# Kernel optimization log

Hardware: AMD Instinct MI355X
Metric: run time of the kernel (lower is better)

Reference implementation:

```python
import jax, jax.numpy as jnp
import numpy as np

B, N, E, F, FE = 4, 10000, 160000, 128, 16  # batch, nodes, edges, filters(=node feat dim), edge feat dim
EPS = 1e-3  # keras LayerNormalization default epsilon


def layernorm(x, gamma, beta):
    mu = jnp.mean(x, axis=-1, keepdims=True)
    var = jnp.mean(jnp.square(x - mu), axis=-1, keepdims=True)
    return (x - mu) * jax.lax.rsqrt(var + EPS) * gamma + beta


def setup_inputs() -> dict:
    key = jax.random.key(0)
    ks = jax.random.split(key, 8)
    nodes = jax.random.normal(ks[0], (B, N, F), dtype=jnp.float32)
    edge_features = jax.random.normal(ks[1], (B, E, FE), dtype=jnp.float32)
    edges = jax.random.randint(ks[2], (B, E, 2), 0, N, dtype=jnp.int32)
    edge_weights = jax.random.uniform(ks[3], (B, E, 1), dtype=jnp.float32)
    edge_dropout = jnp.ones((B, E, 2), dtype=jnp.float32)
    W_msg = jax.random.normal(ks[4], (2 * F + FE, F), dtype=jnp.float32) * 0.02
    b_msg = jnp.zeros((F,), jnp.float32)
    g_msg = jnp.ones((F,), jnp.float32)
    beta_msg = jnp.zeros((F,), jnp.float32)
    W_upd = jax.random.normal(ks[5], (2 * F, F), dtype=jnp.float32) * 0.02
    b_upd = jnp.zeros((F,), jnp.float32)
    g_upd = jnp.ones((F,), jnp.float32)
    beta_upd = jnp.zeros((F,), jnp.float32)
    return dict(nodes=nodes, edge_features=edge_features, edges=edges,
                edge_weights=edge_weights, edge_dropout=edge_dropout,
                W_msg=W_msg, b_msg=b_msg, g_msg=g_msg, beta_msg=beta_msg,
                W_upd=W_upd, b_upd=b_upd, g_upd=g_upd, beta_upd=beta_upd)


def reference(nodes, edge_features, edges, edge_weights, edge_dropout,
              W_msg, b_msg, g_msg, beta_msg, W_upd, b_upd, g_upd, beta_upd):
    n = nodes.shape[1]
    # gather both endpoints per edge: [B,E,2,F] -> [B,E,2F]
    gathered = jax.vmap(lambda nd, ed: nd[ed])(nodes, edges)
    msg_in = gathered.reshape(gathered.shape[0], gathered.shape[1], -1)
    msg_in = jnp.concatenate([msg_in, edge_features], axis=-1)
    # message MLP: Dense + GELU + LayerNorm
    h = jnp.einsum('bei,io->beo', msg_in, W_msg) + b_msg
    messages = layernorm(jax.nn.gelu(h, approximate=False), g_msg, beta_msg)
    weighted_messages = messages * edge_weights
    # scatter-sum to destination nodes (edge[:,1]), masked by dropout col 1
    dropped = weighted_messages * edge_dropout[..., 1:2]
    dst = edges[..., 1]
    aggregated = jax.vmap(lambda m, d: jax.ops.segment_sum(m, d, num_segments=n))(dropped, dst)
    # update: concat + Dense + GELU + LayerNorm
    combined = jnp.concatenate([nodes, aggregated], axis=-1)
    u = jnp.einsum('bni,io->bno', combined, W_upd) + b_upd
    updated_nodes = layernorm(jax.nn.gelu(u, approximate=False), g_upd, beta_upd)
    return updated_nodes
```

## Files before the change

kernel.cpp:

```cpp
#include <hip/hip_runtime.h>
#include <hip/hip_bf16.h>
#include <hip/hip_fp16.h>

#define BATCH   4
#define NNODES  10000
#define NEDGES  160000
#define FDIM    128
#define FEDIM   16
#define LNEPS   1e-3f
#define NTOTE   (BATCH * NEDGES)
#define NTOTN   (BATCH * NNODES)

typedef __attribute__((ext_vector_type(8))) short v8s;
typedef __attribute__((ext_vector_type(4))) float v4f;

#define AGG_BYTES   ((size_t)NTOTN * FDIM * 2)
#define CNT_OFF     AGG_BYTES
#define CNT_BYTES   ((size_t)NTOTN * 4)
#define CUR_OFF     (CNT_OFF + CNT_BYTES)
#define P_OFF       (CUR_OFF + CNT_BYTES)
#define P_BYTES     ((size_t)NTOTN * 256 * 2)
#define WTCAT_OFF   (P_OFF + P_BYTES)
#define WTUPD_OFF   (WTCAT_OFF + (size_t)256 * 128 * 2)
#define W3T_OFF     (WTUPD_OFF + (size_t)128 * 256 * 2)
#define REC_OFF     (W3T_OFF + (size_t)128 * 32 * 2)

static __device__ __forceinline__ unsigned short f2bf(float f) {
    __hip_bfloat16 h = __float2bfloat16(f);
    return *reinterpret_cast<unsigned short*>(&h);
}
static __device__ __forceinline__ float bfbits2f(unsigned bits16) {
    return __uint_as_float(bits16 << 16);
}

static __device__ __forceinline__ float gelu_f(float x) {
    float z = 0.7978845608028654f * (x + 0.044715f * x * x * x);
    float e = __expf(2.0f * z);
    float t = 1.0f - 2.0f / (e + 1.0f);
    return 0.5f * x * (1.0f + t);
}

static __device__ __forceinline__ bool is_bf16_mode(const void* gflag) {
    return ((*reinterpret_cast<const unsigned*>(gflag)) & 0xFFFFu) != 0u;
}
static __device__ __forceinline__ float ld_f(const void* p, long i, bool bf) {
    return bf ? (float)reinterpret_cast<const __hip_bfloat16*>(p)[i]
              : reinterpret_cast<const float*>(p)[i];
}
static __device__ __forceinline__ uint4 pack8(const float* p) {
    float4 f0 = *reinterpret_cast<const float4*>(p);
    float4 f1 = *reinterpret_cast<const float4*>(p + 4);
    uint4 o;
    o.x = f2bf(f0.x) | ((unsigned)f2bf(f0.y) << 16);
    o.y = f2bf(f0.z) | ((unsigned)f2bf(f0.w) << 16);
    o.z = f2bf(f1.x) | ((unsigned)f2bf(f1.y) << 16);
    o.w = f2bf(f1.z) | ((unsigned)f2bf(f1.w) << 16);
    return o;
}
static __device__ __forceinline__ uint4 h8_to_bf8(uint4 u) {
    unsigned w[4] = {u.x, u.y, u.z, u.w};
    uint4 o; unsigned r[4];
    #pragma unroll
    for (int q = 0; q < 4; q++) {
        __half lo = *reinterpret_cast<const __half*>(&w[q]);
        unsigned short hib = (unsigned short)(w[q] >> 16);
        __half hi = *reinterpret_cast<const __half*>(&hib);
        r[q] = f2bf(__half2float(lo)) | ((unsigned)f2bf(__half2float(hi)) << 16);
    }
    o.x = r[0]; o.y = r[1]; o.z = r[2]; o.w = r[3];
    return o;
}
static __device__ __forceinline__ uint4 shfl4(uint4 v, int src) {
    uint4 o;
    o.x = (unsigned)__shfl((int)v.x, src);
    o.y = (unsigned)__shfl((int)v.y, src);
    o.z = (unsigned)__shfl((int)v.z, src);
    o.w = (unsigned)__shfl((int)v.w, src);
    return o;
}

#define NCAT (256 * 128)
#define NUPD (128 * 256)
#define NW3  (128 * 32)
__global__ __launch_bounds__(256) void init_kernel(
    const void* __restrict__ Wmsg, const void* __restrict__ Wupd,
    const void* __restrict__ gflag,
    unsigned short* __restrict__ WtCat,
    unsigned short* __restrict__ WtUpd,
    unsigned short* __restrict__ W3t,
    uint4* __restrict__ aggz,
    uint4* __restrict__ cntz) {
    bool bf = is_bf16_mode(gflag);
    int i = blockIdx.x * 256 + threadIdx.x;
    aggz[i] = make_uint4(0, 0, 0, 0);
    if (i < (int)(CNT_BYTES / 16)) cntz[i] = make_uint4(0, 0, 0, 0);
    if (i < NCAT) {
        int n = i >> 7, k = i & 127;
        int src = (n < 128) ? (k * 128 + n) : ((128 + k) * 128 + (n - 128));
        WtCat[i] = bf ? reinterpret_cast<const unsigned short*>(Wmsg)[src]
                      : f2bf(reinterpret_cast<const float*>(Wmsg)[src]);
    } else if (i < NCAT + NUPD) {
        int j = i - NCAT;
        int n = j >> 8, c = j & 255;
        WtUpd[j] = bf ? reinterpret_cast<const unsigned short*>(Wupd)[c * 128 + n]
                      : f2bf(reinterpret_cast<const float*>(Wupd)[c * 128 + n]);
    } else if (i < NCAT + NUPD + NW3) {
        int j = i - NCAT - NUPD;
        int n = j >> 5, k = j & 31;
        W3t[j] = (k < 16) ? (bf ? reinterpret_cast<const unsigned short*>(Wmsg)[(256 + k) * 128 + n]
                                : f2bf(reinterpret_cast<const float*>(Wmsg)[(256 + k) * 128 + n]))
                          : (unsigned short)0;
    }
}

__global__ __launch_bounds__(1024) void scan_kernel(const int* __restrict__ counts,
                                                    int* __restrict__ cursor) {
    __shared__ int wsum[16];
    const int C = 40;
    int tid = threadIdx.x, lane = tid & 63, wave = tid >> 6;
    int lo = tid * C;
    const bool act = (lo < NTOTN);
    int vals[C];
    int s = 0;
    if (act) {
        #pragma unroll
        for (int q = 0; q < C / 4; q++) {
            int4 t4 = *reinterpret_cast<const int4*>(counts + lo + q * 4);
            vals[q * 4 + 0] = t4.x; vals[q * 4 + 1] = t4.y;
            vals[q * 4 + 2] = t4.z; vals[q * 4 + 3] = t4.w;
            s += t4.x + t4.y + t4.z + t4.w;
        }
    }
    int sc = s;
    #pragma unroll
    for (int off = 1; off < 64; off <<= 1) {
        int v = __shfl_up(sc, off);
        if (lane >= off) sc += v;
    }
    if (lane == 63) wsum[wave] = sc;
    __syncthreads();
    if (wave == 0 && lane < 16) {
        int t = wsum[lane];
        #pragma unroll
        for (int off = 1; off < 16; off <<= 1) {
            int v = __shfl_up(t, off);
            if (lane >= off) t += v;
        }
        wsum[lane] = t;
    }
    __syncthreads();
    int run = (wave > 0 ? wsum[wave - 1] : 0) + (sc - s);
    if (act) {
        #pragma unroll
        for (int q = 0; q < C / 4; q++) {
            int4 o;
            o.x = run; run += vals[q * 4 + 0];
            o.y = run; run += vals[q * 4 + 1];
            o.z = run; run += vals[q * 4 + 2];
            o.w = run; run += vals[q * 4 + 3];
            *reinterpret_cast<int4*>(cursor + lo + q * 4) = o;
        }
    }
}

__global__ __launch_bounds__(256) void sort_scatter(
    const int*  __restrict__ edges,
    const void* __restrict__ ew,
    const void* __restrict__ ed,
    const void* __restrict__ efeat,
    const void* __restrict__ gflag,
    int*        __restrict__ cursor,
    uint4*      __restrict__ rec4)
{
    const bool bf = is_bf16_mode(gflag);
    int gid = blockIdx.x * 256 + threadIdx.x;
    const int lane = threadIdx.x & 63, k = lane & 3, g4 = lane & ~3;
    int b = gid / NEDGES;
    long be = gid;
    int2 e = reinterpret_cast<const int2*>(edges)[gid];
    float w = ld_f(ew, be, bf) * ld_f(ed, be * 2 + 1, bf);
    uint4 R0, R1;
    if (bf) {
        const unsigned short* ep = reinterpret_cast<const unsigned short*>(efeat) + be * FEDIM;
        R0 = *reinterpret_cast<const uint4*>(ep);
        R1 = *reinterpret_cast<const uint4*>(ep + 8);
    } else {
        const float* ep = reinterpret_cast<const float*>(efeat) + be * FEDIM;
        R0 = pack8(ep);
        R1 = pack8(ep + 8);
    }
    uint4 R2 = make_uint4((unsigned)(b * NNODES + e.x),
                          (unsigned)(b * NNODES + e.y),
                          __float_as_uint(w),
                          (unsigned)gid);
    int pos = atomicAdd(&cursor[b * NNODES + e.y], 1);

    #pragma unroll
    for (int j = 0; j < 4; j++) {
        int src = g4 + j;
        uint4 a0 = shfl4(R0, src);
        uint4 a1 = shfl4(R1, src);
        uint4 a2 = shfl4(R2, src);
        int   pj = __shfl(pos, src);
        uint4 wv = (k == 0) ? a0 : (k == 1) ? a1 : (k == 2) ? a2 : make_uint4(0, 0, 0, 0);
        rec4[(size_t)pj * 4 + k] = wv;
    }
}

__global__ __launch_bounds__(256) void pg_kernel(
    const void* __restrict__ nodes,
    const void* __restrict__ bmsg,
    const void* __restrict__ gflag,
    const unsigned short* __restrict__ Wt,
    const int*  __restrict__ edges,
    int*        __restrict__ counts,
    unsigned short*       __restrict__ P)
{
    const bool bf = is_bf16_mode(gflag);
    __shared__ unsigned short sW[128 * 40];
    __shared__ unsigned short sA[128 * 40];

    const int tid  = threadIdx.x;
    const int lane = tid & 63, wave = tid >> 6;
    const int c    = lane & 15, quad = lane >> 4;
    const int row0 = blockIdx.x * 128;
    const int half = blockIdx.y;
    const int NROWS = BATCH * NNODES;

    if (half == 0) {
        #pragma unroll
        for (int k = 0; k < 8; k++) {
            int g = blockIdx.x * 2048 + k * 256 + tid;
            if (g < NTOTE) {
                int2 e = reinterpret_cast<const int2*>(edges)[g];
                atomicAdd(&counts[(g / NEDGES) * NNODES + e.y], 1);
            }
        }
    }

    float bcol[8];
    #pragma unroll
    for (int nt = 0; nt < 8; nt++)
        bcol[nt] = (half == 0) ? ld_f(bmsg, nt * 16 + c, bf) : 0.f;

    v4f acc[2][8];
    #pragma unroll
    for (int mt = 0; mt < 2; mt++)
        #pragma unroll
        for (int nt = 0; nt < 8; nt++) { v4f z = {0.f, 0.f, 0.f, 0.f}; acc[mt][nt] = z; }

    for (int ks = 0; ks < 4; ks++) {
        #pragma unroll
        for (int q = tid; q < 512; q += 256) {
            int n = q >> 2, part = q & 3;
            *reinterpret_cast<uint4*>(&sW[n * 40 + part * 8]) =
                *reinterpret_cast<const uint4*>(Wt + (half * 128 + n) * 128 + ks * 32 + part * 8);
        }
        #pragma unroll
        for (int q = tid; q < 512; q += 256) {
            int t = q >> 2, part = q & 3;
            int row = row0 + t; if (row >= NROWS) row = NROWS - 1;
            long off = (size_t)row * FDIM + ks * 32 + part * 8;
            uint4 v = bf ? *reinterpret_cast<const uint4*>(reinterpret_cast<const unsigned short*>(nodes) + off)
                         : pack8(reinterpret_cast<const float*>(nodes) + off);
            *reinterpret_cast<uint4*>(&sA[t * 40 + part * 8]) = v;
        }
        __syncthreads();

        v8s a0 = *reinterpret_cast<const v8s*>(&sA[(wave * 32 + c) * 40 + quad * 8]);
        v8s a1 = *reinterpret_cast<const v8s*>(&sA[(wave * 32 + 16 + c) * 40 + quad * 8]);
        #pragma unroll
        for (int nt = 0; nt < 8; nt++) {
            v8s bfr = *reinterpret_cast<const v8s*>(&sW[(nt * 16 + c) * 40 + quad * 8]);
            acc[0][nt] = __builtin_amdgcn_mfma_f32_16x16x32_bf16(a0, bfr, acc[0][nt], 0, 0, 0);
            acc[1][nt] = __builtin_amdgcn_mfma_f32_16x16x32_bf16(a1, bfr, acc[1][nt], 0, 0, 0);
        }
        __syncthreads();
    }

    #pragma unroll
    for (int mt = 0; mt < 2; mt++)
        #pragma unroll
        for (int r = 0; r < 4; r++) {
            int row = row0 + wave * 32 + mt * 16 + quad * 4 + r;
            if (row < NROWS) {
                float v[8];
                #pragma unroll
                for (int nt = 0; nt < 8; nt++) v[nt] = acc[mt][nt][r] + bcol[nt];
                uint4 o;
                o.x = f2bf(v[0]) | ((unsigned)f2bf(v[1]) << 16);
                o.y = f2bf(v[2]) | ((unsigned)f2bf(v[3]) << 16);
                o.z = f2bf(v[4]) | ((unsigned)f2bf(v[5]) << 16);
                o.w = f2bf(v[6]) | ((unsigned)f2bf(v[7]) << 16);
                *reinterpret_cast<uint4*>(P + (size_t)row * 256 + half * 128 + c * 8) = o;
            }
        }
}

__global__ __launch_bounds__(256) void edge_kernel(
    const unsigned short* __restrict__ P,
    const uint4*          __restrict__ rec4,
    const unsigned short* __restrict__ W3t,
    const void* __restrict__ gmsg,
    const void* __restrict__ betamsg,
    __half*     __restrict__ agg)
{
    const bool bf = is_bf16_mode(gmsg);
    const int tid  = threadIdx.x;
    const int lane = tid & 63, wave = tid >> 6;
    const int c    = lane & 15, quad = lane >> 4;
    const int we0  = blockIdx.x * 128 + wave * 32;

    float gcol[8], becol[8];
    #pragma unroll
    for (int nt = 0; nt < 8; nt++) {
        gcol[nt]  = ld_f(gmsg, nt * 16 + c, bf);
        becol[nt] = ld_f(betamsg, nt * 16 + c, bf);
    }

    v8s bfrag[8];
    #pragma unroll
    for (int nt = 0; nt < 8; nt++)
        bfrag[nt] = *reinterpret_cast<const v8s*>(W3t + (nt * 16 + c) * 32 + quad * 8);

    v4f acc[2][8];
    #pragma unroll
    for (int mt = 0; mt < 2; mt++)
        #pragma unroll
        for (int nt = 0; nt < 8; nt++) { v4f z = {0.f, 0.f, 0.f, 0.f}; acc[mt][nt] = z; }

    #pragma unroll
    for (int mt = 0; mt < 2; mt++) {
        v8s a = {0, 0, 0, 0, 0, 0, 0, 0};
        if (quad < 2) {
            int slot = we0 + ((c >> 2) << 3) + mt * 4 + (c & 3);
            uint4 u = rec4[(size_t)slot * 4 + quad];
            a = *reinterpret_cast<v8s*>(&u);
        }
        #pragma unroll
        for (int nt = 0; nt < 8; nt++)
            acc[mt][nt] = __builtin_amdgcn_mfma_f32_16x16x32_bf16(a, bfrag[nt], acc[mt][nt], 0, 0, 0);
    }

    const bool even = !(c & 1);
    float racc[8];
    int cur = -1;

    auto flushv = [&](int dstrow) {
        __half* aout = agg + (size_t)dstrow * FDIM;
        #pragma unroll
        for (int np = 0; np < 4; np++) {
            int nt = np * 2;
            float t0 = __shfl_xor(racc[nt], 1);
            float t1 = __shfl_xor(racc[nt + 1], 1);
            __half2 v = even ? __floats2half2_rn(racc[nt], t0)
                             : __floats2half2_rn(t1, racc[nt + 1]);
            int hoff = even ? (nt * 16 + c) : ((nt + 1) * 16 + c - 1);
            unsafeAtomicAdd(reinterpret_cast<__half2*>(aout + hoff), v);
        }
    };

    #pragma unroll
    for (int mt = 0; mt < 2; mt++) {
        uint4 H[4];
        #pragma unroll
        for (int r = 0; r < 4; r++)
            H[r] = rec4[(size_t)(we0 + quad * 8 + mt * 4 + r) * 4 + 2];
        uint4 U1[4], U2[4];
        #pragma unroll
        for (int r = 0; r < 4; r++) {
            U1[r] = *reinterpret_cast<const uint4*>(P + (size_t)H[r].x * 256 + c * 8);
            U2[r] = *reinterpret_cast<const uint4*>(P + (size_t)H[r].y * 256 + 128 + c * 8);
        }
        #pragma unroll
        for (int r = 0; r < 4; r++) {
            unsigned w1[4] = {U1[r].x, U1[r].y, U1[r].z, U1[r].w};
            unsigned w2[4] = {U2[r].x, U2[r].y, U2[r].z, U2[r].w};
            float h[8];
            #pragma unroll
            for (int q = 0; q < 4; q++) {
                h[q * 2]     = bfbits2f(w1[q] & 0xFFFFu) + bfbits2f(w2[q] & 0xFFFFu) + acc[mt][q * 2][r];
                h[q * 2 + 1] = __uint_as_float(w1[q] & 0xFFFF0000u) + __uint_as_float(w2[q] & 0xFFFF0000u)
                               + acc[mt][q * 2 + 1][r];
            }
            float s = 0.f, sq = 0.f;
            #pragma unroll
            for (int nt = 0; nt < 8; nt++) {
                float g = gelu_f(h[nt]);
                h[nt] = g; s += g; sq += g * g;
            }
            #pragma unroll
            for (int off = 1; off < 16; off <<= 1) {
                s  += __shfl_xor(s, off);
                sq += __shfl_xor(sq, off);
            }
            float mu  = s * (1.0f / 128.0f);
            float var = sq * (1.0f / 128.0f) - mu * mu;
            float rs  = rsqrtf(var + LNEPS);
            float wgt = __uint_as_float(H[r].z);
            int d = (int)H[r].y;
            if (d != cur) {
                if (cur >= 0) flushv(cur);
                cur = d;
                #pragma unroll
                for (int nt = 0; nt < 8; nt++)
                    racc[nt] = ((h[nt] - mu) * rs * gcol[nt] + becol[nt]) * wgt;
            } else {
                #pragma unroll
                for (int nt = 0; nt < 8; nt++)
                    racc[nt] += ((h[nt] - mu) * rs * gcol[nt] + becol[nt]) * wgt;
            }
        }
    }
    flushv(cur);
}

__global__ __launch_bounds__(256) void upd_kernel(
    const void* __restrict__ nodes,
    const __half* __restrict__ agg,
    const unsigned short* __restrict__ Wt,
    const void* __restrict__ bupd,
    const void* __restrict__ gupd,
    const void* __restrict__ beupd,
    void*       __restrict__ out)
{
    const bool bf = is_bf16_mode(gupd);
    __shared__ unsigned short sW[128 * 40];
    __shared__ unsigned short sA[64 * 40];

    const int tid  = threadIdx.x;
    const int lane = tid & 63, wave = tid >> 6;
    const int c    = lane & 15, quad = lane >> 4;
    const int row0 = blockIdx.x * 64;

    float bcol[8], gcol[8], becol[8];
    #pragma unroll
    for (int nt = 0; nt < 8; nt++) {
        int col = nt * 16 + c;
        bcol[nt]  = ld_f(bupd, col, bf);
        gcol[nt]  = ld_f(gupd, col, bf);
        becol[nt] = ld_f(beupd, col, bf);
    }

    v4f acc[8];
    #pragma unroll
    for (int nt = 0; nt < 8; nt++) { v4f z = {0.f, 0.f, 0.f, 0.f}; acc[nt] = z; }

    for (int ks = 0; ks < 8; ks++) {
        #pragma unroll
        for (int q = tid; q < 512; q += 256) {
            int n = q >> 2, part = q & 3;
            *reinterpret_cast<uint4*>(&sW[n * 40 + part * 8]) =
                *reinterpret_cast<const uint4*>(Wt + n * 256 + ks * 32 + part * 8);
        }
        {
            int t = tid >> 2, part = tid & 3;
            int row = row0 + t;
            uint4 v;
            if (ks < 4) {
                long off = (size_t)row * FDIM + ks * 32 + part * 8;
                v = bf ? *reinterpret_cast<const uint4*>(reinterpret_cast<const unsigned short*>(nodes) + off)
                       : pack8(reinterpret_cast<const float*>(nodes) + off);
            } else {
                uint4 u = *reinterpret_cast<const uint4*>(
                    reinterpret_cast<const unsigned short*>(agg) + (size_t)row * FDIM + (ks - 4) * 32 + part * 8);
                v = h8_to_bf8(u);
            }
            *reinterpret_cast<uint4*>(&sA[t * 40 + part * 8]) = v;
        }
        __syncthreads();

        v8s a0 = *reinterpret_cast<const v8s*>(&sA[(wave * 16 + c) * 40 + quad * 8]);
        #pragma unroll
        for (int nt = 0; nt < 8; nt++) {
            v8s bfr = *reinterpret_cast<const v8s*>(&sW[(nt * 16 + c) * 40 + quad * 8]);
            acc[nt] = __builtin_amdgcn_mfma_f32_16x16x32_bf16(a0, bfr, acc[nt], 0, 0, 0);
        }
        __syncthreads();
    }

    float s[4] = {0, 0, 0, 0}, sq[4] = {0, 0, 0, 0};
    #pragma unroll
    for (int nt = 0; nt < 8; nt++) {
        v4f v = acc[nt];
        #pragma unroll
        for (int r = 0; r < 4; r++) {
            float g = gelu_f(v[r] + bcol[nt]);
            v[r] = g;
            s[r] += g; sq[r] += g * g;
        }
        acc[nt] = v;
    }
    #pragma unroll
    for (int off = 1; off < 16; off <<= 1) {
        #pragma unroll
        for (int r = 0; r < 4; r++) {
            s[r]  += __shfl_xor(s[r], off);
            sq[r] += __shfl_xor(sq[r], off);
        }
    }
    #pragma unroll
    for (int r = 0; r < 4; r++) {
        float mu  = s[r] * (1.0f / 128.0f);
        float var = sq[r] * (1.0f / 128.0f) - mu * mu;
        float rs  = rsqrtf(var + LNEPS);
        int row = row0 + wave * 16 + quad * 4 + r;
        #pragma unroll
        for (int nt = 0; nt < 8; nt++) {
            float y = (acc[nt][r] - mu) * rs * gcol[nt] + becol[nt];
            size_t oi = (size_t)row * FDIM + nt * 16 + c;
            if (bf) reinterpret_cast<__hip_bfloat16*>(out)[oi] = __float2bfloat16(y);
            else    reinterpret_cast<float*>(out)[oi] = y;
        }
    }
}

extern "C" void kernel_launch(void* const* d_in, const int* in_sizes, int n_in,
                              void* d_out, int out_size, void* d_ws, size_t ws_size,
                              hipStream_t stream)
{
    const void* nodes   = d_in[0];
    const void* efeat   = d_in[1];
    const int*  edges   = (const int*)d_in[2];
    const void* ew      = d_in[3];
    const void* ed      = d_in[4];
    const void* Wmsg    = d_in[5];
    const void* bmsg    = d_in[6];
    const void* gmsg    = d_in[7];
    const void* betamsg = d_in[8];
    const void* Wupd    = d_in[9];
    const void* bupd    = d_in[10];
    const void* gupd    = d_in[11];
    const void* betaupd = d_in[12];

    char* ws = (char*)d_ws;
    __half* agg          = (__half*)ws;
    int*    counts       = (int*)(ws + CNT_OFF);
    int*    cursor       = (int*)(ws + CUR_OFF);
    unsigned short* P    = (unsigned short*)(ws + P_OFF);
    unsigned short* WtCat= (unsigned short*)(ws + WTCAT_OFF);
    unsigned short* WtUpd= (unsigned short*)(ws + WTUPD_OFF);
    unsigned short* W3t  = (unsigned short*)(ws + W3T_OFF);
    uint4*          rec4 = (uint4*)(ws + REC_OFF);

    init_kernel<<<2500, 256, 0, stream>>>(
        Wmsg, Wupd, gmsg, WtCat, WtUpd, W3t, (uint4*)agg, (uint4*)counts);
    pg_kernel<<<dim3(313, 2), 256, 0, stream>>>(
        nodes, bmsg, gmsg, WtCat, edges, counts, P);
    scan_kernel<<<1, 1024, 0, stream>>>(counts, cursor);
    sort_scatter<<<NTOTE / 256, 256, 0, stream>>>(
        edges, ew, ed, efeat, gmsg, cursor, rec4);
    edge_kernel<<<NTOTE / 128, 256, 0, stream>>>(
        P, rec4, W3t, gmsg, betamsg, agg);
    upd_kernel<<<NTOTN / 64, 256, 0, stream>>>(
        nodes, agg, WtUpd, bupd, gupd, betaupd, d_out);
}
```

Measured before the change: 321.6 us.

## Spread per-node counters four ways, enlarge edge tiles, skip atomics for owned rows

Node counts and cursors are split into four sub-counters per destination node, chosen by thread index, so the counting and sort atomics in pg_kernel and sort_scatter contend less. sort_scatter now writes records directly instead of shuffling them across lanes. edge_kernel handles 512 edges per block, with each quad walking 32 consecutive sorted edges, and uses plain stores instead of atomic adds when a destination run lies entirely inside one quad's range. GELU and rsqrt switch to cheaper rcp/rsq builtins. The scan grows to four times as many entries and rereads its counts instead of caching them in registers; the init_kernel zeroing covers the larger buffer only if its grid is big enough.

```diff
diff --git a/kernel.cpp b/kernel.cpp
--- a/kernel.cpp
+++ b/kernel.cpp
@@ -16,7 +16,7 @@
 
 #define AGG_BYTES   ((size_t)NTOTN * FDIM * 2)
 #define CNT_OFF     AGG_BYTES
-#define CNT_BYTES   ((size_t)NTOTN * 4)
+#define CNT_BYTES   ((size_t)NTOTN * 4 * 4)
 #define CUR_OFF     (CNT_OFF + CNT_BYTES)
 #define P_OFF       (CUR_OFF + CNT_BYTES)
 #define P_BYTES     ((size_t)NTOTN * 256 * 2)
@@ -34,10 +34,11 @@
 }
 
 static __device__ __forceinline__ float gelu_f(float x) {
-    float z = 0.7978845608028654f * (x + 0.044715f * x * x * x);
-    float e = __expf(2.0f * z);
-    float t = 1.0f - 2.0f / (e + 1.0f);
-    return 0.5f * x * (1.0f + t);
+    float x2 = x * x;
+    float z2 = 1.5957691216f * x * __builtin_fmaf(0.044715f, x2, 1.0f);
+    float e  = __expf(z2);
+    float r  = __builtin_amdgcn_rcpf(e + 1.0f);
+    return __builtin_fmaf(-x, r, x);
 }
 
 static __device__ __forceinline__ bool is_bf16_mode(const void* gflag) {
@@ -68,14 +69,6 @@
         r[q] = f2bf(__half2float(lo)) | ((unsigned)f2bf(__half2float(hi)) << 16);
     }
     o.x = r[0]; o.y = r[1]; o.z = r[2]; o.w = r[3];
-    return o;
-}
-static __device__ __forceinline__ uint4 shfl4(uint4 v, int src) {
-    uint4 o;
-    o.x = (unsigned)__shfl((int)v.x, src);
-    o.y = (unsigned)__shfl((int)v.y, src);
-    o.z = (unsigned)__shfl((int)v.z, src);
-    o.w = (unsigned)__shfl((int)v.w, src);
     return o;
 }
 
@@ -113,21 +106,18 @@
     }
 }
 
-__global__ __launch_bounds__(1024) void scan_kernel(const int* __restrict__ counts,
-                                                    int* __restrict__ cursor) {
+__global__ __launch_bounds__(1024) void scan_kernel(const int* __restrict__ counts4,
+                                                    int* __restrict__ cursor4) {
     __shared__ int wsum[16];
-    const int C = 40;
+    const int N4 = NTOTN * 4;
+    const int C = 160;
     int tid = threadIdx.x, lane = tid & 63, wave = tid >> 6;
     int lo = tid * C;
-    const bool act = (lo < NTOTN);
-    int vals[C];
+    const bool act = (lo < N4);
     int s = 0;
     if (act) {
-        #pragma unroll
         for (int q = 0; q < C / 4; q++) {
-            int4 t4 = *reinterpret_cast<const int4*>(counts + lo + q * 4);
-            vals[q * 4 + 0] = t4.x; vals[q * 4 + 1] = t4.y;
-            vals[q * 4 + 2] = t4.z; vals[q * 4 + 3] = t4.w;
+            int4 t4 = *reinterpret_cast<const int4*>(counts4 + lo + q * 4);
             s += t4.x + t4.y + t4.z + t4.w;
         }
     }
@@ -151,14 +141,14 @@
     __syncthreads();
     int run = (wave > 0 ? wsum[wave - 1] : 0) + (sc - s);
     if (act) {
-        #pragma unroll
         for (int q = 0; q < C / 4; q++) {
+            int4 t4 = *reinterpret_cast<const int4*>(counts4 + lo + q * 4);
             int4 o;
-            o.x = run; run += vals[q * 4 + 0];
-            o.y = run; run += vals[q * 4 + 1];
-            o.z = run; run += vals[q * 4 + 2];
-            o.w = run; run += vals[q * 4 + 3];
-            *reinterpret_cast<int4*>(cursor + lo + q * 4) = o;
+            o.x = run; run += t4.x;
+            o.y = run; run += t4.y;
+            o.z = run; run += t4.z;
+            o.w = run; run += t4.w;
+            *reinterpret_cast<int4*>(cursor4 + lo + q * 4) = o;
         }
     }
 }
@@ -169,12 +159,11 @@
     const void* __restrict__ ed,
     const void* __restrict__ efeat,
     const void* __restrict__ gflag,
-    int*        __restrict__ cursor,
+    int*        __restrict__ cursor4,
     uint4*      __restrict__ rec4)
 {
     const bool bf = is_bf16_mode(gflag);
     int gid = blockIdx.x * 256 + threadIdx.x;
-    const int lane = threadIdx.x & 63, k = lane & 3, g4 = lane & ~3;
     int b = gid / NEDGES;
     long be = gid;
     int2 e = reinterpret_cast<const int2*>(edges)[gid];
@@ -189,22 +178,14 @@
         R0 = pack8(ep);
         R1 = pack8(ep + 8);
     }
-    uint4 R2 = make_uint4((unsigned)(b * NNODES + e.x),
-                          (unsigned)(b * NNODES + e.y),
-                          __float_as_uint(w),
-                          (unsigned)gid);
-    int pos = atomicAdd(&cursor[b * NNODES + e.y], 1);
-
-    #pragma unroll
-    for (int j = 0; j < 4; j++) {
-        int src = g4 + j;
-        uint4 a0 = shfl4(R0, src);
-        uint4 a1 = shfl4(R1, src);
-        uint4 a2 = shfl4(R2, src);
-        int   pj = __shfl(pos, src);
-        uint4 wv = (k == 0) ? a0 : (k == 1) ? a1 : (k == 2) ? a2 : make_uint4(0, 0, 0, 0);
-        rec4[(size_t)pj * 4 + k] = wv;
-    }
+    int pos = atomicAdd(&cursor4[((size_t)b * NNODES + e.y) * 4 + (threadIdx.x & 3)], 1);
+    uint4* rp = rec4 + (size_t)pos * 4;
+    rp[0] = R0;
+    rp[1] = R1;
+    rp[2] = make_uint4((unsigned)(b * NNODES + e.x),
+                       (unsigned)(b * NNODES + e.y),
+                       __float_as_uint(w), (unsigned)gid);
+    rp[3] = make_uint4(0, 0, 0, 0);
 }
 
 __global__ __launch_bounds__(256) void pg_kernel(
@@ -213,7 +194,7 @@
     const void* __restrict__ gflag,
     const unsigned short* __restrict__ Wt,
     const int*  __restrict__ edges,
-    int*        __restrict__ counts,
+    int*        __restrict__ counts4,
     unsigned short*       __restrict__ P)
 {
     const bool bf = is_bf16_mode(gflag);
@@ -233,7 +214,7 @@
             int g = blockIdx.x * 2048 + k * 256 + tid;
             if (g < NTOTE) {
                 int2 e = reinterpret_cast<const int2*>(edges)[g];
-                atomicAdd(&counts[(g / NEDGES) * NNODES + e.y], 1);
+                atomicAdd(&counts4[((size_t)(g / NEDGES) * NNODES + e.y) * 4 + (tid & 3)], 1);
             }
         }
     }
@@ -309,7 +290,8 @@
     const int tid  = threadIdx.x;
     const int lane = tid & 63, wave = tid >> 6;
     const int c    = lane & 15, quad = lane >> 4;
-    const int we0  = blockIdx.x * 128 + wave * 32;
+    const int wbase = blockIdx.x * 512 + wave * 128;
+    const int q0    = wbase + quad * 32;
 
     float gcol[8], becol[8];
     #pragma unroll
@@ -323,30 +305,15 @@
     for (int nt = 0; nt < 8; nt++)
         bfrag[nt] = *reinterpret_cast<const v8s*>(W3t + (nt * 16 + c) * 32 + quad * 8);
 
-    v4f acc[2][8];
-    #pragma unroll
-    for (int mt = 0; mt < 2; mt++)
-        #pragma unroll
-        for (int nt = 0; nt < 8; nt++) { v4f z = {0.f, 0.f, 0.f, 0.f}; acc[mt][nt] = z; }
-
-    #pragma unroll
-    for (int mt = 0; mt < 2; mt++) {
-        v8s a = {0, 0, 0, 0, 0, 0, 0, 0};
-        if (quad < 2) {
-            int slot = we0 + ((c >> 2) << 3) + mt * 4 + (c & 3);
-            uint4 u = rec4[(size_t)slot * 4 + quad];
-            a = *reinterpret_cast<v8s*>(&u);
-        }
-        #pragma unroll
-        for (int nt = 0; nt < 8; nt++)
-            acc[mt][nt] = __builtin_amdgcn_mfma_f32_16x16x32_bf16(a, bfrag[nt], acc[mt][nt], 0, 0, 0);
-    }
+    const int prevd = (q0 == 0) ? -1 : (int)rec4[(size_t)(q0 - 1) * 4 + 2].y;
+    const int nextd = (q0 + 32 >= NTOTE) ? -1 : (int)rec4[(size_t)(q0 + 32) * 4 + 2].y;
 
     const bool even = !(c & 1);
     float racc[8];
-    int cur = -1;
-
-    auto flushv = [&](int dstrow) {
+    int  cur = -1;
+    bool owned = true;
+
+    auto flushv = [&](int dstrow, bool plain) {
         __half* aout = agg + (size_t)dstrow * FDIM;
         #pragma unroll
         for (int np = 0; np < 4; np++) {
@@ -356,63 +323,86 @@
             __half2 v = even ? __floats2half2_rn(racc[nt], t0)
                              : __floats2half2_rn(t1, racc[nt + 1]);
             int hoff = even ? (nt * 16 + c) : ((nt + 1) * 16 + c - 1);
-            unsafeAtomicAdd(reinterpret_cast<__half2*>(aout + hoff), v);
+            if (plain) *reinterpret_cast<__half2*>(aout + hoff) = v;
+            else       unsafeAtomicAdd(reinterpret_cast<__half2*>(aout + hoff), v);
         }
     };
 
-    #pragma unroll
-    for (int mt = 0; mt < 2; mt++) {
-        uint4 H[4];
-        #pragma unroll
-        for (int r = 0; r < 4; r++)
-            H[r] = rec4[(size_t)(we0 + quad * 8 + mt * 4 + r) * 4 + 2];
-        uint4 U1[4], U2[4];
-        #pragma unroll
-        for (int r = 0; r < 4; r++) {
-            U1[r] = *reinterpret_cast<const uint4*>(P + (size_t)H[r].x * 256 + c * 8);
-            U2[r] = *reinterpret_cast<const uint4*>(P + (size_t)H[r].y * 256 + 128 + c * 8);
-        }
-        #pragma unroll
-        for (int r = 0; r < 4; r++) {
-            unsigned w1[4] = {U1[r].x, U1[r].y, U1[r].z, U1[r].w};
-            unsigned w2[4] = {U2[r].x, U2[r].y, U2[r].z, U2[r].w};
-            float h[8];
+    for (int g = 0; g < 4; g++) {
+        v4f acc[2][8];
+        #pragma unroll
+        for (int mt = 0; mt < 2; mt++)
             #pragma unroll
-            for (int q = 0; q < 4; q++) {
-                h[q * 2]     = bfbits2f(w1[q] & 0xFFFFu) + bfbits2f(w2[q] & 0xFFFFu) + acc[mt][q * 2][r];
-                h[q * 2 + 1] = __uint_as_float(w1[q] & 0xFFFF0000u) + __uint_as_float(w2[q] & 0xFFFF0000u)
-                               + acc[mt][q * 2 + 1][r];
-            }
-            float s = 0.f, sq = 0.f;
-            #pragma unroll
-            for (int nt = 0; nt < 8; nt++) {
-                float g = gelu_f(h[nt]);
-                h[nt] = g; s += g; sq += g * g;
+            for (int nt = 0; nt < 8; nt++) { v4f z = {0.f, 0.f, 0.f, 0.f}; acc[mt][nt] = z; }
+
+        #pragma unroll
+        for (int mt = 0; mt < 2; mt++) {
+            v8s a = {0, 0, 0, 0, 0, 0, 0, 0};
+            if (quad < 2) {
+                int slot = wbase + (c >> 2) * 32 + g * 8 + mt * 4 + (c & 3);
+                uint4 u = rec4[(size_t)slot * 4 + quad];
+                a = *reinterpret_cast<v8s*>(&u);
             }
             #pragma unroll
-            for (int off = 1; off < 16; off <<= 1) {
-                s  += __shfl_xor(s, off);
-                sq += __shfl_xor(sq, off);
+            for (int nt = 0; nt < 8; nt++)
+                acc[mt][nt] = __builtin_amdgcn_mfma_f32_16x16x32_bf16(a, bfrag[nt], acc[mt][nt], 0, 0, 0);
+        }
+
+        #pragma unroll
+        for (int mt = 0; mt < 2; mt++) {
+            uint4 H[4];
+            #pragma unroll
+            for (int r = 0; r < 4; r++)
+                H[r] = rec4[(size_t)(q0 + g * 8 + mt * 4 + r) * 4 + 2];
+            uint4 U1[4], U2[4];
+            #pragma unroll
+            for (int r = 0; r < 4; r++) {
+                U1[r] = *reinterpret_cast<const uint4*>(P + (size_t)H[r].x * 256 + c * 8);
+                U2[r] = *reinterpret_cast<const uint4*>(P + (size_t)H[r].y * 256 + 128 + c * 8);
             }
-            float mu  = s * (1.0f / 128.0f);
-            float var = sq * (1.0f / 128.0f) - mu * mu;
-            float rs  = rsqrtf(var + LNEPS);
-            float wgt = __uint_as_float(H[r].z);
-            int d = (int)H[r].y;
-            if (d != cur) {
-                if (cur >= 0) flushv(cur);
-                cur = d;
+            #pragma unroll
+            for (int r = 0; r < 4; r++) {
+                unsigned w1[4] = {U1[r].x, U1[r].y, U1[r].z, U1[r].w};
+                unsigned w2[4] = {U2[r].x, U2[r].y, U2[r].z, U2[r].w};
+                float h[8];
                 #pragma unroll
-                for (int nt = 0; nt < 8; nt++)
-                    racc[nt] = ((h[nt] - mu) * rs * gcol[nt] + becol[nt]) * wgt;
-            } else {
+                for (int q = 0; q < 4; q++) {
+                    h[q * 2]     = bfbits2f(w1[q] & 0xFFFFu) + bfbits2f(w2[q] & 0xFFFFu) + acc[mt][q * 2][r];
+                    h[q * 2 + 1] = __uint_as_float(w1[q] & 0xFFFF0000u) + __uint_as_float(w2[q] & 0xFFFF0000u)
+                                   + acc[mt][q * 2 + 1][r];
+                }
+                float s = 0.f, sq = 0.f;
                 #pragma unroll
-                for (int nt = 0; nt < 8; nt++)
-                    racc[nt] += ((h[nt] - mu) * rs * gcol[nt] + becol[nt]) * wgt;
+                for (int nt = 0; nt < 8; nt++) {
+                    float gg = gelu_f(h[nt]);
+                    h[nt] = gg; s += gg; sq += gg * gg;
+                }
+                #pragma unroll
+                for (int off = 1; off < 16; off <<= 1) {
+                    s  += __shfl_xor(s, off);
+                    sq += __shfl_xor(sq, off);
+                }
+                float mu  = s * (1.0f / 128.0f);
+                float var = sq * (1.0f / 128.0f) - mu * mu;
+                float rs  = __builtin_amdgcn_rsqf(var + LNEPS);
+                float wgt = __uint_as_float(H[r].z);
+                int d = (int)H[r].y;
+                if (d != cur) {
+                    if (cur >= 0) { flushv(cur, owned); owned = true; }
+                    else owned = (d != prevd);
+                    cur = d;
+                    #pragma unroll
+                    for (int nt = 0; nt < 8; nt++)
+                        racc[nt] = ((h[nt] - mu) * rs * gcol[nt] + becol[nt]) * wgt;
+                } else {
+                    #pragma unroll
+                    for (int nt = 0; nt < 8; nt++)
+                        racc[nt] += ((h[nt] - mu) * rs * gcol[nt] + becol[nt]) * wgt;
+                }
             }
         }
     }
-    flushv(cur);
+    flushv(cur, owned && (cur != nextd));
 }
 
 __global__ __launch_bounds__(256) void upd_kernel(
@@ -503,7 +493,7 @@
     for (int r = 0; r < 4; r++) {
         float mu  = s[r] * (1.0f / 128.0f);
         float var = sq[r] * (1.0f / 128.0f) - mu * mu;
-        float rs  = rsqrtf(var + LNEPS);
+        float rs  = __builtin_amdgcn_rsqf(var + LNEPS);
         int row = row0 + wave * 16 + quad * 4 + r;
         #pragma unroll
         for (int nt = 0; nt < 8; nt++) {
@@ -535,8 +525,8 @@
 
     char* ws = (char*)d_ws;
     __half* agg          = (__half*)ws;
-    int*    counts       = (int*)(ws + CNT_OFF);
-    int*    cursor       = (int*)(ws + CUR_OFF);
+    int*    counts4      = (int*)(ws + CNT_OFF);
+    int*    cursor4      = (int*)(ws + CUR_OFF);
     unsigned short* P    = (unsigned short*)(ws + P_OFF);
     unsigned short* WtCat= (unsigned short*)(ws + WTCAT_OFF);
     unsigned short* WtUpd= (unsigned short*)(ws + WTUPD_OFF);
@@ -544,13 +534,13 @@
     uint4*          rec4 = (uint4*)(ws + REC_OFF);
 
     init_kernel<<<2500, 256, 0, stream>>>(
-        Wmsg, Wupd, gmsg, WtCat, WtUpd, W3t, (uint4*)agg, (uint4*)counts);
+        Wmsg, Wupd, gmsg, WtCat, WtUpd, W3t, (uint4*)agg, (uint4*)counts4);
     pg_kernel<<<dim3(313, 2), 256, 0, stream>>>(
-        nodes, bmsg, gmsg, WtCat, edges, counts, P);
-    scan_kernel<<<1, 1024, 0, stream>>>(counts, cursor);
+        nodes, bmsg, gmsg, WtCat, edges, counts4, P);
+    scan_kernel<<<1, 1024, 0, stream>>>(counts4, cursor4);
     sort_scatter<<<NTOTE / 256, 256, 0, stream>>>(
-        edges, ew, ed, efeat, gmsg, cursor, rec4);
-    edge_kernel<<<NTOTE / 128, 256, 0, stream>>>(
+        edges, ew, ed, efeat, gmsg, cursor4, rec4);
+    edge_kernel<<<NTOTE / 512, 256, 0, stream>>>(
         P, rec4, W3t, gmsg, betamsg, agg);
     upd_kernel<<<NTOTN / 64, 256, 0, stream>>>(
         nodes, agg, WtUpd, bupd, gupd, betaupd, d_out);
```

Result: slower. 357.3 us (+11.1%).

## Give each lane group a longer sorted edge run and use plain stores for owned segments

Applied to the files above, without the earlier changes.

The edge kernel now has each 16-lane group process 32 consecutive sorted edges in 8 phases instead of 8 edges, with fewer blocks. Destination segments that begin and end inside the group's range are written with plain stores, not atomics, by checking the neighbouring records' destination ids. The GELU is rewritten with fma and a hardware reciprocal, rsqrt uses the amdgcn intrinsic, and sort_scatter skips writing the unused fourth record slot. This trades atomic traffic and instruction count for less parallelism and a serial phase loop per wave.

```diff
diff --git a/kernel.cpp b/kernel.cpp
--- a/kernel.cpp
+++ b/kernel.cpp
@@ -34,10 +34,11 @@
 }
 
 static __device__ __forceinline__ float gelu_f(float x) {
-    float z = 0.7978845608028654f * (x + 0.044715f * x * x * x);
-    float e = __expf(2.0f * z);
-    float t = 1.0f - 2.0f / (e + 1.0f);
-    return 0.5f * x * (1.0f + t);
+    float x2 = x * x;
+    float z2 = 1.5957691216f * x * __builtin_fmaf(0.044715f, x2, 1.0f);
+    float e  = __expf(z2);
+    float r  = __builtin_amdgcn_rcpf(e + 1.0f);
+    return __builtin_fmaf(-x, r, x);
 }
 
 static __device__ __forceinline__ bool is_bf16_mode(const void* gflag) {
@@ -202,8 +203,10 @@
         uint4 a1 = shfl4(R1, src);
         uint4 a2 = shfl4(R2, src);
         int   pj = __shfl(pos, src);
-        uint4 wv = (k == 0) ? a0 : (k == 1) ? a1 : (k == 2) ? a2 : make_uint4(0, 0, 0, 0);
-        rec4[(size_t)pj * 4 + k] = wv;
+        if (k < 3) {
+            uint4 wv = (k == 0) ? a0 : (k == 1) ? a1 : a2;
+            rec4[(size_t)pj * 4 + k] = wv;
+        }
     }
 }
 
@@ -309,7 +312,8 @@
     const int tid  = threadIdx.x;
     const int lane = tid & 63, wave = tid >> 6;
     const int c    = lane & 15, quad = lane >> 4;
-    const int we0  = blockIdx.x * 128 + wave * 32;
+    const int wbase = blockIdx.x * 512 + wave * 128;
+    const int q0    = wbase + quad * 32;
 
     float gcol[8], becol[8];
     #pragma unroll
@@ -323,30 +327,15 @@
     for (int nt = 0; nt < 8; nt++)
         bfrag[nt] = *reinterpret_cast<const v8s*>(W3t + (nt * 16 + c) * 32 + quad * 8);
 
-    v4f acc[2][8];
-    #pragma unroll
-    for (int mt = 0; mt < 2; mt++)
-        #pragma unroll
-        for (int nt = 0; nt < 8; nt++) { v4f z = {0.f, 0.f, 0.f, 0.f}; acc[mt][nt] = z; }
-
-    #pragma unroll
-    for (int mt = 0; mt < 2; mt++) {
-        v8s a = {0, 0, 0, 0, 0, 0, 0, 0};
-        if (quad < 2) {
-            int slot = we0 + ((c >> 2) << 3) + mt * 4 + (c & 3);
-            uint4 u = rec4[(size_t)slot * 4 + quad];
-            a = *reinterpret_cast<v8s*>(&u);
-        }
-        #pragma unroll
-        for (int nt = 0; nt < 8; nt++)
-            acc[mt][nt] = __builtin_amdgcn_mfma_f32_16x16x32_bf16(a, bfrag[nt], acc[mt][nt], 0, 0, 0);
-    }
+    const int prevd = (q0 == 0) ? -1 : (int)rec4[(size_t)(q0 - 1) * 4 + 2].y;
+    const int nextd = (q0 + 32 >= NTOTE) ? -1 : (int)rec4[(size_t)(q0 + 32) * 4 + 2].y;
 
     const bool even = !(c & 1);
     float racc[8];
-    int cur = -1;
-
-    auto flushv = [&](int dstrow) {
+    int  cur = -1;
+    bool owned = true;
+
+    auto flushv = [&](int dstrow, bool plain) {
         __half* aout = agg + (size_t)dstrow * FDIM;
         #pragma unroll
         for (int np = 0; np < 4; np++) {
@@ -356,16 +345,30 @@
             __half2 v = even ? __floats2half2_rn(racc[nt], t0)
                              : __floats2half2_rn(t1, racc[nt + 1]);
             int hoff = even ? (nt * 16 + c) : ((nt + 1) * 16 + c - 1);
-            unsafeAtomicAdd(reinterpret_cast<__half2*>(aout + hoff), v);
+            if (plain) *reinterpret_cast<__half2*>(aout + hoff) = v;
+            else       unsafeAtomicAdd(reinterpret_cast<__half2*>(aout + hoff), v);
         }
     };
 
-    #pragma unroll
-    for (int mt = 0; mt < 2; mt++) {
+    #pragma unroll 1
+    for (int ph = 0; ph < 8; ph++) {
+        v8s a = {0, 0, 0, 0, 0, 0, 0, 0};
+        if (quad < 2) {
+            int slot = wbase + (c >> 2) * 32 + ph * 4 + (c & 3);
+            uint4 u = rec4[(size_t)slot * 4 + quad];
+            a = *reinterpret_cast<v8s*>(&u);
+        }
+        v4f acc[8];
+        #pragma unroll
+        for (int nt = 0; nt < 8; nt++) { v4f z = {0.f, 0.f, 0.f, 0.f}; acc[nt] = z; }
+        #pragma unroll
+        for (int nt = 0; nt < 8; nt++)
+            acc[nt] = __builtin_amdgcn_mfma_f32_16x16x32_bf16(a, bfrag[nt], acc[nt], 0, 0, 0);
+
         uint4 H[4];
         #pragma unroll
         for (int r = 0; r < 4; r++)
-            H[r] = rec4[(size_t)(we0 + quad * 8 + mt * 4 + r) * 4 + 2];
+            H[r] = rec4[(size_t)(q0 + ph * 4 + r) * 4 + 2];
         uint4 U1[4], U2[4];
         #pragma unroll
         for (int r = 0; r < 4; r++) {
@@ -379,15 +382,15 @@
             float h[8];
             #pragma unroll
             for (int q = 0; q < 4; q++) {
-                h[q * 2]     = bfbits2f(w1[q] & 0xFFFFu) + bfbits2f(w2[q] & 0xFFFFu) + acc[mt][q * 2][r];
+                h[q * 2]     = bfbits2f(w1[q] & 0xFFFFu) + bfbits2f(w2[q] & 0xFFFFu) + acc[q * 2][r];
                 h[q * 2 + 1] = __uint_as_float(w1[q] & 0xFFFF0000u) + __uint_as_float(w2[q] & 0xFFFF0000u)
-                               + acc[mt][q * 2 + 1][r];
+                               + acc[q * 2 + 1][r];
             }
             float s = 0.f, sq = 0.f;
             #pragma unroll
             for (int nt = 0; nt < 8; nt++) {
-                float g = gelu_f(h[nt]);
-                h[nt] = g; s += g; sq += g * g;
+                float gg = gelu_f(h[nt]);
+                h[nt] = gg; s += gg; sq += gg * gg;
             }
             #pragma unroll
             for (int off = 1; off < 16; off <<= 1) {
@@ -396,11 +399,12 @@
             }
             float mu  = s * (1.0f / 128.0f);
             float var = sq * (1.0f / 128.0f) - mu * mu;
-            float rs  = rsqrtf(var + LNEPS);
+            float rs  = __builtin_amdgcn_rsqf(var + LNEPS);
             float wgt = __uint_as_float(H[r].z);
             int d = (int)H[r].y;
             if (d != cur) {
-                if (cur >= 0) flushv(cur);
+                if (cur >= 0) { flushv(cur, owned); owned = true; }
+                else owned = (d != prevd);
                 cur = d;
                 #pragma unroll
                 for (int nt = 0; nt < 8; nt++)
@@ -412,7 +416,7 @@
             }
         }
     }
-    flushv(cur);
+    flushv(cur, owned && (cur != nextd));
 }
 
 __global__ __launch_bounds__(256) void upd_kernel(
@@ -503,7 +507,7 @@
     for (int r = 0; r < 4; r++) {
         float mu  = s[r] * (1.0f / 128.0f);
         float var = sq[r] * (1.0f / 128.0f) - mu * mu;
-        float rs  = rsqrtf(var + LNEPS);
+        float rs  = __builtin_amdgcn_rsqf(var + LNEPS);
         int row = row0 + wave * 16 + quad * 4 + r;
         #pragma unroll
         for (int nt = 0; nt < 8; nt++) {
@@ -550,7 +554,7 @@
     scan_kernel<<<1, 1024, 0, stream>>>(counts, cursor);
     sort_scatter<<<NTOTE / 256, 256, 0, stream>>>(
         edges, ew, ed, efeat, gmsg, cursor, rec4);
-    edge_kernel<<<NTOTE / 128, 256, 0, stream>>>(
+    edge_kernel<<<NTOTE / 512, 256, 0, stream>>>(
         P, rec4, W3t, gmsg, betamsg, agg);
     upd_kernel<<<NTOTN / 64, 256, 0, stream>>>(
         nodes, agg, WtUpd, bupd, gupd, betaupd, d_out);
```

Measured after the change: 301.4 us. 6.3% less time.
